# Performance work log

Measured on AMD Instinct MI355X. Metric: run time of the kernel, lower is better.

The kernel has to match this reference:

```python
import jax, jax.numpy as jnp
import numpy as np

N = 200000  # num nodes == num edges (edge_weight serves as both node feature and edge weight)
D_HID = 128
D_OUT = 2


def setup_inputs() -> dict:
    key = jax.random.key(0)
    ks = jax.random.split(key, 5)
    edge_index = jax.random.randint(ks[0], (2, N), 0, N, dtype=jnp.int64)
    edge_weight = jax.random.uniform(ks[1], (N,), dtype=jnp.float32)
    # Glorot-ish init for GCNConv linear layers (bias=True by default in PyG)
    W1 = jax.random.normal(ks[2], (1, D_HID), dtype=jnp.float32) * (1.0 / np.sqrt(1))
    W2 = jax.random.normal(ks[3], (D_HID, D_HID), dtype=jnp.float32) * (1.0 / np.sqrt(D_HID))
    W3 = jax.random.normal(ks[4], (D_HID, D_OUT), dtype=jnp.float32) * (1.0 / np.sqrt(D_HID))
    b1 = jnp.zeros((D_HID,), dtype=jnp.float32)
    b2 = jnp.zeros((D_HID,), dtype=jnp.float32)
    b3 = jnp.zeros((D_OUT,), dtype=jnp.float32)
    return {"edge_index": edge_index, "edge_weight": edge_weight,
            "W1": W1, "b1": b1, "W2": W2, "b2": b2, "W3": W3, "b3": b3}


def reference(edge_index, edge_weight, W1, b1, W2, b2, W3, b3):
    n = edge_weight.shape[0]
    src, dst = edge_index[0], edge_index[1]
    # GCN symmetric normalization with self-loops (PyG gcn_norm, fill_value=1.0)
    loops = jnp.arange(n)
    src_f = jnp.concatenate([src, loops])            # [2N]
    dst_f = jnp.concatenate([dst, loops])            # [2N]
    w_f = jnp.concatenate([edge_weight, jnp.ones((n,), edge_weight.dtype)])
    deg = jax.ops.segment_sum(w_f, dst_f, num_segments=n)
    dinv = jnp.where(deg > 0, deg ** -0.5, 0.0)
    norm = dinv[src_f] * w_f * dinv[dst_f]           # [2N], identical for all layers

    def conv(x, W, b):
        h = x @ W                                    # linear transform first (out <= in path)
        msg = h[src_f] * norm[:, None]               # gather + edge scale
        return jax.ops.segment_sum(msg, dst_f, num_segments=n) + b  # scatter-add aggregate

    x = edge_weight[:, None]                         # node features = edge weights, [N,1]
    x = jax.nn.relu(conv(x, W1, b1))
    x = jax.nn.relu(conv(x, W2, b2))
    x = jax.nn.relu(conv(x, W3, b3))
    return jax.nn.log_softmax(x, axis=1)
```

## Files before the change

### kernel.cpp

```cpp
#include <hip/hip_runtime.h>

#define NN 200000
#define NE 200000
#define DH 128

typedef float f32x4 __attribute__((ext_vector_type(4)));
typedef _Float16 f16x8 __attribute__((ext_vector_type(8)));
#define AS1 __attribute__((address_space(1)))
#define AS3 __attribute__((address_space(3)))

__device__ __forceinline__ unsigned pack2h(float a, float b) {
  unsigned short ua = __builtin_bit_cast(unsigned short, (_Float16)a);
  unsigned short ub = __builtin_bit_cast(unsigned short, (_Float16)b);
  return (unsigned)ua | ((unsigned)ub << 16);
}

__global__ void k_deg(const int* __restrict__ dst, const float* __restrict__ ew,
                      int* __restrict__ pdeg, int* __restrict__ rank,
                      const float* __restrict__ W2, unsigned* __restrict__ w2g) {
  int tid = threadIdx.x;
  int e = blockIdx.x * 256 + tid;
  if (e < NE) {
    int d = dst[e];
    int addend = __float2int_rn(ew[e] * 1048576.0f) | (1 << 26);
    int old = atomicAdd(&pdeg[d], addend);
    rank[e] = (int)(((unsigned)old) >> 26);
  }
  if (blockIdx.x < 32) {
    int gid = blockIdx.x * 256 + tid;
    int fkc = gid >> 8, l = (gid >> 2) & 63, dd = gid & 3;
    int n = (fkc >> 2) * 16 + (l & 15);
    int dwp = (fkc & 3) * 16 + (l >> 4) * 4 + dd;
    w2g[gid] = pack2h(W2[(2 * dwp) * DH + n], W2[(2 * dwp + 1) * DH + n]);
  }
}

__global__ void k_scan1(const int* __restrict__ pdeg, int* __restrict__ rowptr,
                        int* __restrict__ bsum) {
  __shared__ int sm[256];
  int tid = threadIdx.x;
  int i = blockIdx.x * 256 + tid;
  int v = (i < NN) ? (int)(((unsigned)pdeg[i]) >> 26) : 0;
  sm[tid] = v;
  __syncthreads();
  int x = v;
  for (int off = 1; off < 256; off <<= 1) {
    int y = (tid >= off) ? sm[tid - off] : 0;
    __syncthreads();
    x += y;
    sm[tid] = x;
    __syncthreads();
  }
  if (i < NN) rowptr[i] = x - v;
  if (tid == 255) bsum[blockIdx.x] = x;
}

__global__ void k_scan3(int* __restrict__ rowptr, const int* __restrict__ bsum,
                        const int* __restrict__ pdeg, const float* __restrict__ ew,
                        float* __restrict__ dinv, float* __restrict__ s) {
  __shared__ int sm[256];
  int tid = threadIdx.x;
  int partial = 0;
  for (int b = tid; b < blockIdx.x; b += 256) partial += bsum[b];
  sm[tid] = partial;
  __syncthreads();
  for (int off = 128; off; off >>= 1) {
    if (tid < off) sm[tid] += sm[tid + off];
    __syncthreads();
  }
  int boff = sm[0];
  int i = blockIdx.x * 256 + tid;
  if (i < NN) {
    rowptr[i] += boff;
    float deg = (float)(((unsigned)pdeg[i]) & 0x03FFFFFFu) * (1.0f / 1048576.0f) + 1.0f;
    float dv = rsqrtf(deg);
    dinv[i] = dv;
    s[i] = dv * dv * ew[i];
  }
  if (i == 0) rowptr[NN] = NE;
}

__global__ void k_scatter(const int* __restrict__ src, const int* __restrict__ dst,
                          const float* __restrict__ ew, const int* __restrict__ rank,
                          const float* __restrict__ dinv, const int* __restrict__ rowptr,
                          float* __restrict__ s, int2* __restrict__ epack) {
  int e = blockIdx.x * 256 + threadIdx.x;
  if (e < NE) {
    int si = src[e], di = dst[e];
    float nr = dinv[si] * ew[e] * dinv[di];
    int pos = rowptr[di] + rank[e];
    epack[pos] = make_int2(si, __float_as_int(nr));
    atomicAdd(&s[di], nr * ew[si]);
  }
}

__global__ __launch_bounds__(256, 3) void k_layer2(
    const float* __restrict__ s, const float* __restrict__ dinv,
    const int* __restrict__ rowptr, const int2* __restrict__ epack,
    const float* __restrict__ W1, const float* __restrict__ b1,
    const float* __restrict__ b2, const float* __restrict__ W3,
    const unsigned* __restrict__ w2g, float* __restrict__ h3) {
  __shared__ __align__(16) uint4 tAf[1024];
  __shared__ __align__(16) unsigned w2t[8192];
  __shared__ float eS[256], eN[256];
  int tid = threadIdx.x;
  int wv = tid >> 6;

#pragma unroll
  for (int i = 0; i < 8; ++i)
    __builtin_amdgcn_global_load_lds(
        (const AS1 unsigned*)(w2g + i * 1024 + tid * 4),
        (AS3 unsigned*)(w2t + i * 1024 + wv * 256), 16, 0, 0);

  int base = blockIdx.x * 64;
  int lr15 = tid & 15, q = (tid >> 4) & 3;
  int d = base + wv * 16 + lr15;
  float w1r[32], b1r[32];
#pragma unroll
  for (int c = 0; c < 32; c++) { w1r[c] = W1[q * 32 + c]; b1r[c] = b1[q * 32 + c]; }

  float sd = s[d], dv = dinv[d], sn = dv * dv;
  float acc[32];
#pragma unroll
  for (int c = 0; c < 32; c++)
    acc[c] = sn * fmaxf(fmaf(sd, w1r[c], b1r[c]), 0.f);

  int begd = rowptr[d], endd = rowptr[d + 1];
  int beg = rowptr[base], end = rowptr[base + 64];

  for (int cb = beg; cb < end; cb += 256) {
    int ce = min(cb + 256, end);
    __syncthreads();
    if (tid < ce - cb) {
      int2 ep = epack[cb + tid];
      eS[tid] = s[ep.x];
      eN[tid] = __int_as_float(ep.y);
    }
    __syncthreads();
    int jb = max(begd, cb), je = min(endd, ce);
    for (int j = jb; j < je; ++j) {
      float ss = eS[j - cb], nr = eN[j - cb];
#pragma unroll
      for (int c = 0; c < 32; c++)
        acc[c] = fmaf(nr, fmaxf(fmaf(ss, w1r[c], b1r[c]), 0.f), acc[c]);
    }
  }

#pragma unroll
  for (int hi = 0; hi < 4; ++hi) {
    uint4 u;
    u.x = pack2h(acc[8 * hi + 0], acc[8 * hi + 1]);
    u.y = pack2h(acc[8 * hi + 2], acc[8 * hi + 3]);
    u.z = pack2h(acc[8 * hi + 4], acc[8 * hi + 5]);
    u.w = pack2h(acc[8 * hi + 6], acc[8 * hi + 7]);
    tAf[(wv * 4 + q) * 64 + hi * 16 + lr15] = u;
  }
  __syncthreads();

  int l = tid & 63, g = l >> 4, lr = l & 15;
  f32x4 acc8[8];
#pragma unroll
  for (int f = 0; f < 8; f++) acc8[f] = (f32x4){0.f, 0.f, 0.f, 0.f};
#pragma unroll
  for (int kc = 0; kc < 4; kc++) {
    f16x8 av = __builtin_bit_cast(f16x8, tAf[(wv * 4 + kc) * 64 + l]);
#pragma unroll
    for (int f = 0; f < 8; f++) {
      f16x8 bv = __builtin_bit_cast(f16x8, *(const uint4*)(w2t + ((f * 4 + kc) * 64 + l) * 4));
      acc8[f] = __builtin_amdgcn_mfma_f32_16x16x32_f16(av, bv, acc8[f], 0, 0, 0);
    }
  }

  float p0[4] = {0.f, 0.f, 0.f, 0.f}, p1[4] = {0.f, 0.f, 0.f, 0.f};
#pragma unroll
  for (int f = 0; f < 8; f++) {
    int n = f * 16 + lr;
    float bb = b2[n];
    float2 w3v = ((const float2*)W3)[n];
#pragma unroll
    for (int r = 0; r < 4; r++) {
      float v = fmaxf(acc8[f][r] + bb, 0.f);
      p0[r] = fmaf(v, w3v.x, p0[r]);
      p1[r] = fmaf(v, w3v.y, p1[r]);
    }
  }
#pragma unroll
  for (int r = 0; r < 4; r++) {
#pragma unroll
    for (int m = 8; m; m >>= 1) {
      p0[r] += __shfl_xor(p0[r], m);
      p1[r] += __shfl_xor(p1[r], m);
    }
  }
  if (lr == 0) {
#pragma unroll
    for (int r = 0; r < 4; r++) {
      int node = base + wv * 16 + g * 4 + r;
      ((float2*)h3)[node] = make_float2(p0[r], p1[r]);
    }
  }
}

__global__ void k_final(const float* __restrict__ h3, const float* __restrict__ dinv,
                        const int* __restrict__ rowptr, const int2* __restrict__ epack,
                        const float* __restrict__ b3, float* __restrict__ out) {
  int d = blockIdx.x * 256 + threadIdx.x;
  if (d < NN) {
    float dv = dinv[d], sn = dv * dv;
    float2 hv = ((const float2*)h3)[d];
    float y0 = sn * hv.x, y1 = sn * hv.y;
    int beg = rowptr[d], end = rowptr[d + 1];
    for (int j = beg; j < end; ++j) {
      int2 ep = epack[j];
      float2 hs = ((const float2*)h3)[ep.x];
      float nr = __int_as_float(ep.y);
      y0 = fmaf(nr, hs.x, y0);
      y1 = fmaf(nr, hs.y, y1);
    }
    float z0 = fmaxf(y0 + b3[0], 0.f);
    float z1 = fmaxf(y1 + b3[1], 0.f);
    float m = fmaxf(z0, z1);
    float lse = m + logf(expf(z0 - m) + expf(z1 - m));
    out[2 * d] = z0 - lse;
    out[2 * d + 1] = z1 - lse;
  }
}

extern "C" void kernel_launch(void* const* d_in, const int* in_sizes, int n_in,
                              void* d_out, int out_size, void* d_ws, size_t ws_size,
                              hipStream_t stream) {
  const int* ei = (const int*)d_in[0];
  const int* srcp = ei;
  const int* dstp = ei + NE;
  const float* ew = (const float*)d_in[1];
  const float* W1 = (const float*)d_in[2];
  const float* b1 = (const float*)d_in[3];
  const float* W2 = (const float*)d_in[4];
  const float* b2 = (const float*)d_in[5];
  const float* W3 = (const float*)d_in[6];
  const float* b3 = (const float*)d_in[7];
  float* out = (float*)d_out;

  char* ws = (char*)d_ws;
  size_t off = 0;
  auto alloc = [&](size_t bytes) -> void* {
    void* p = ws + off;
    off = (off + bytes + 255) & ~size_t(255);
    return p;
  };
  int* pdeg = (int*)alloc(NN * 4);
  size_t zero_bytes = off;
  int* rank = (int*)alloc(NE * 4);
  float* s = (float*)alloc(NN * 4);
  float* dinv = (float*)alloc(NN * 4);
  int* rowptr = (int*)alloc((NN + 1) * 4);
  int* bsum = (int*)alloc(1024 * 4);
  int2* epack = (int2*)alloc(NE * 8);
  unsigned* w2g = (unsigned*)alloc(8192 * 4);
  float* h3 = (float*)alloc(NN * 2 * 4);
  (void)ws_size; (void)in_sizes; (void)n_in; (void)out_size;

  const int nbE = (NE + 255) / 256;
  const int nbN = (NN + 255) / 256;

  hipMemsetAsync(pdeg, 0, zero_bytes, stream);
  k_deg<<<nbE, 256, 0, stream>>>(dstp, ew, pdeg, rank, W2, w2g);
  k_scan1<<<nbN, 256, 0, stream>>>(pdeg, rowptr, bsum);
  k_scan3<<<nbN, 256, 0, stream>>>(rowptr, bsum, pdeg, ew, dinv, s);
  k_scatter<<<nbE, 256, 0, stream>>>(srcp, dstp, ew, rank, dinv, rowptr, s, epack);
  k_layer2<<<NN / 64, 256, 0, stream>>>(s, dinv, rowptr, epack, W1, b1, b2, W3, w2g, h3);
  k_final<<<nbN, 256, 0, stream>>>(h3, dinv, rowptr, epack, b3, out);
}
```

Measured before the change: 135.4 us.

## Fuse pipeline into one cooperative persistent kernel with grid syncs and tile tickets

Replaces the six-kernel chain (degree, two scan passes, scatter, layer2, final) with one cooperative kernel. It uses grid-wide syncs between phases and an atomic ticket for dynamic tile scheduling in the MFMA layer. The aim is to remove launch overhead and inter-kernel gaps on the mostly small phases. The cost is grid.sync overhead, a grid capped at 3 blocks per CU, and a naive per-chunk block-offset reduction in the scan phase that runs in quadratic time. The old multi-kernel path is kept as a fallback if the cooperative launch fails.

```diff
diff --git a/kernel.cpp b/kernel.cpp
--- a/kernel.cpp
+++ b/kernel.cpp
@@ -1,8 +1,13 @@
 #include <hip/hip_runtime.h>
+#include <hip/hip_cooperative_groups.h>
 
 #define NN 200000
 #define NE 200000
 #define DH 128
+#define NTILES (NN / 64)
+#define NCH ((NN + 255) / 256)
+
+namespace cg = cooperative_groups;
 
 typedef float f32x4 __attribute__((ext_vector_type(4)));
 typedef _Float16 f16x8 __attribute__((ext_vector_type(8)));
@@ -13,6 +18,216 @@
   unsigned short ua = __builtin_bit_cast(unsigned short, (_Float16)a);
   unsigned short ub = __builtin_bit_cast(unsigned short, (_Float16)b);
   return (unsigned)ua | ((unsigned)ub << 16);
+}
+
+__global__ __launch_bounds__(256, 3) void k_all(
+    const int* __restrict__ src, const int* __restrict__ dst,
+    const float* __restrict__ ew,
+    const float* __restrict__ W1, const float* __restrict__ b1,
+    const float* __restrict__ W2, const float* __restrict__ b2,
+    const float* __restrict__ W3, const float* __restrict__ b3,
+    float* __restrict__ out,
+    int* __restrict__ pdeg, int* __restrict__ ticket, int* __restrict__ rank,
+    float* __restrict__ s, float* __restrict__ dinv, int* __restrict__ rowptr,
+    int* __restrict__ agg, int2* __restrict__ epack,
+    unsigned* __restrict__ w2g, float* __restrict__ h3) {
+  cg::grid_group grid = cg::this_grid();
+  __shared__ __align__(16) char smem[51200];
+  uint4* tAf = (uint4*)smem;
+  unsigned* w2t = (unsigned*)(smem + 16384);
+  float* eS = (float*)(smem + 49152);
+  float* eN = (float*)(smem + 50176);
+  int* sm = (int*)smem;
+  __shared__ int s_tile;
+  int tid = threadIdx.x;
+  int gsz = gridDim.x * 256;
+  int gtid = blockIdx.x * 256 + tid;
+
+  for (int e = gtid; e < NE; e += gsz) {
+    int d = dst[e];
+    int addend = __float2int_rn(ew[e] * 1048576.0f) | (1 << 26);
+    int old = atomicAdd(&pdeg[d], addend);
+    rank[e] = (int)(((unsigned)old) >> 26);
+  }
+  for (int gid = gtid; gid < 8192; gid += gsz) {
+    int fkc = gid >> 8, l = (gid >> 2) & 63, dd = gid & 3;
+    int n = (fkc >> 2) * 16 + (l & 15);
+    int dwp = (fkc & 3) * 16 + (l >> 4) * 4 + dd;
+    w2g[gid] = pack2h(W2[(2 * dwp) * DH + n], W2[(2 * dwp + 1) * DH + n]);
+  }
+  grid.sync();
+
+  for (int c = blockIdx.x; c < NCH; c += gridDim.x) {
+    int i = c * 256 + tid;
+    int v = (i < NN) ? (int)(((unsigned)pdeg[i]) >> 26) : 0;
+    __syncthreads();
+    sm[tid] = v;
+    __syncthreads();
+    int x = v;
+    for (int off = 1; off < 256; off <<= 1) {
+      int y = (tid >= off) ? sm[tid - off] : 0;
+      __syncthreads();
+      x += y;
+      sm[tid] = x;
+      __syncthreads();
+    }
+    if (i < NN) rowptr[i] = x - v;
+    if (tid == 255) agg[c] = x;
+  }
+  grid.sync();
+
+  for (int c = blockIdx.x; c < NCH; c += gridDim.x) {
+    int partial = 0;
+    for (int j = tid; j < c; j += 256) partial += agg[j];
+    __syncthreads();
+    sm[tid] = partial;
+    __syncthreads();
+    for (int off = 128; off; off >>= 1) {
+      if (tid < off) sm[tid] += sm[tid + off];
+      __syncthreads();
+    }
+    int boff = sm[0];
+    int i = c * 256 + tid;
+    if (i < NN) {
+      rowptr[i] += boff;
+      float deg = (float)(((unsigned)pdeg[i]) & 0x03FFFFFFu) * (1.0f / 1048576.0f) + 1.0f;
+      float dv = rsqrtf(deg);
+      dinv[i] = dv;
+      s[i] = dv * dv * ew[i];
+    }
+  }
+  if (gtid == 0) rowptr[NN] = NE;
+  grid.sync();
+
+  for (int e = gtid; e < NE; e += gsz) {
+    int si = src[e], di = dst[e];
+    float nr = dinv[si] * ew[e] * dinv[di];
+    int pos = rowptr[di] + rank[e];
+    epack[pos] = make_int2(si, __float_as_int(nr));
+    atomicAdd(&s[di], nr * ew[si]);
+  }
+  grid.sync();
+
+  int wv = tid >> 6;
+#pragma unroll
+  for (int i = 0; i < 8; ++i)
+    __builtin_amdgcn_global_load_lds(
+        (const AS1 unsigned*)(w2g + i * 1024 + tid * 4),
+        (AS3 unsigned*)(w2t + i * 1024 + wv * 256), 16, 0, 0);
+  int lr15 = tid & 15, q = (tid >> 4) & 3;
+  float w1r[32], b1r[32];
+#pragma unroll
+  for (int c = 0; c < 32; c++) { w1r[c] = W1[q * 32 + c]; b1r[c] = b1[q * 32 + c]; }
+  int l = tid & 63, g = l >> 4, lr = l & 15;
+
+  for (;;) {
+    if (tid == 0) s_tile = atomicAdd(ticket, 1);
+    __syncthreads();
+    int tile = s_tile;
+    if (tile >= NTILES) break;
+    int base = tile * 64;
+    int d = base + wv * 16 + lr15;
+
+    float sd = s[d], dv = dinv[d], sn = dv * dv;
+    float acc[32];
+#pragma unroll
+    for (int c = 0; c < 32; c++)
+      acc[c] = sn * fmaxf(fmaf(sd, w1r[c], b1r[c]), 0.f);
+
+    int begd = rowptr[d], endd = rowptr[d + 1];
+    int beg = rowptr[base], end = rowptr[base + 64];
+    for (int cb = beg; cb < end; cb += 256) {
+      int ce = min(cb + 256, end);
+      __syncthreads();
+      if (tid < ce - cb) {
+        int2 ep = epack[cb + tid];
+        eS[tid] = s[ep.x];
+        eN[tid] = __int_as_float(ep.y);
+      }
+      __syncthreads();
+      int jb = max(begd, cb), je = min(endd, ce);
+      for (int j = jb; j < je; ++j) {
+        float ss = eS[j - cb], nr = eN[j - cb];
+#pragma unroll
+        for (int c = 0; c < 32; c++)
+          acc[c] = fmaf(nr, fmaxf(fmaf(ss, w1r[c], b1r[c]), 0.f), acc[c]);
+      }
+    }
+
+#pragma unroll
+    for (int hi = 0; hi < 4; ++hi) {
+      uint4 u;
+      u.x = pack2h(acc[8 * hi + 0], acc[8 * hi + 1]);
+      u.y = pack2h(acc[8 * hi + 2], acc[8 * hi + 3]);
+      u.z = pack2h(acc[8 * hi + 4], acc[8 * hi + 5]);
+      u.w = pack2h(acc[8 * hi + 6], acc[8 * hi + 7]);
+      tAf[(wv * 4 + q) * 64 + hi * 16 + lr15] = u;
+    }
+    __syncthreads();
+
+    f32x4 acc8[8];
+#pragma unroll
+    for (int f = 0; f < 8; f++) acc8[f] = (f32x4){0.f, 0.f, 0.f, 0.f};
+#pragma unroll
+    for (int kc = 0; kc < 4; kc++) {
+      f16x8 av = __builtin_bit_cast(f16x8, tAf[(wv * 4 + kc) * 64 + l]);
+#pragma unroll
+      for (int f = 0; f < 8; f++) {
+        f16x8 bv = __builtin_bit_cast(f16x8, *(const uint4*)(w2t + ((f * 4 + kc) * 64 + l) * 4));
+        acc8[f] = __builtin_amdgcn_mfma_f32_16x16x32_f16(av, bv, acc8[f], 0, 0, 0);
+      }
+    }
+
+    float p0[4] = {0.f, 0.f, 0.f, 0.f}, p1[4] = {0.f, 0.f, 0.f, 0.f};
+#pragma unroll
+    for (int f = 0; f < 8; f++) {
+      int n = f * 16 + lr;
+      float bb = b2[n];
+      float2 w3v = ((const float2*)W3)[n];
+#pragma unroll
+      for (int r = 0; r < 4; r++) {
+        float v = fmaxf(acc8[f][r] + bb, 0.f);
+        p0[r] = fmaf(v, w3v.x, p0[r]);
+        p1[r] = fmaf(v, w3v.y, p1[r]);
+      }
+    }
+#pragma unroll
+    for (int r = 0; r < 4; r++) {
+#pragma unroll
+      for (int m = 8; m; m >>= 1) {
+        p0[r] += __shfl_xor(p0[r], m);
+        p1[r] += __shfl_xor(p1[r], m);
+      }
+    }
+    if (lr == 0) {
+#pragma unroll
+      for (int r = 0; r < 4; r++) {
+        int node = base + wv * 16 + g * 4 + r;
+        ((float2*)h3)[node] = make_float2(p0[r], p1[r]);
+      }
+    }
+  }
+  grid.sync();
+
+  for (int d = gtid; d < NN; d += gsz) {
+    float dv = dinv[d], sn = dv * dv;
+    float2 hv = ((const float2*)h3)[d];
+    float y0 = sn * hv.x, y1 = sn * hv.y;
+    int beg = rowptr[d], end = rowptr[d + 1];
+    for (int j = beg; j < end; ++j) {
+      int2 ep = epack[j];
+      float2 hs = ((const float2*)h3)[ep.x];
+      float nr = __int_as_float(ep.y);
+      y0 = fmaf(nr, hs.x, y0);
+      y1 = fmaf(nr, hs.y, y1);
+    }
+    float z0 = fmaxf(y0 + b3[0], 0.f);
+    float z1 = fmaxf(y1 + b3[1], 0.f);
+    float m = fmaxf(z0, z1);
+    float lse = m + logf(expf(z0 - m) + expf(z1 - m));
+    out[2 * d] = z0 - lse;
+    out[2 * d + 1] = z1 - lse;
+  }
 }
 
 __global__ void k_deg(const int* __restrict__ dst, const float* __restrict__ ew,
@@ -105,29 +320,24 @@
   __shared__ float eS[256], eN[256];
   int tid = threadIdx.x;
   int wv = tid >> 6;
-
 #pragma unroll
   for (int i = 0; i < 8; ++i)
     __builtin_amdgcn_global_load_lds(
         (const AS1 unsigned*)(w2g + i * 1024 + tid * 4),
         (AS3 unsigned*)(w2t + i * 1024 + wv * 256), 16, 0, 0);
-
   int base = blockIdx.x * 64;
   int lr15 = tid & 15, q = (tid >> 4) & 3;
   int d = base + wv * 16 + lr15;
   float w1r[32], b1r[32];
 #pragma unroll
   for (int c = 0; c < 32; c++) { w1r[c] = W1[q * 32 + c]; b1r[c] = b1[q * 32 + c]; }
-
   float sd = s[d], dv = dinv[d], sn = dv * dv;
   float acc[32];
 #pragma unroll
   for (int c = 0; c < 32; c++)
     acc[c] = sn * fmaxf(fmaf(sd, w1r[c], b1r[c]), 0.f);
-
   int begd = rowptr[d], endd = rowptr[d + 1];
   int beg = rowptr[base], end = rowptr[base + 64];
-
   for (int cb = beg; cb < end; cb += 256) {
     int ce = min(cb + 256, end);
     __syncthreads();
@@ -145,7 +355,6 @@
         acc[c] = fmaf(nr, fmaxf(fmaf(ss, w1r[c], b1r[c]), 0.f), acc[c]);
     }
   }
-
 #pragma unroll
   for (int hi = 0; hi < 4; ++hi) {
     uint4 u;
@@ -156,7 +365,6 @@
     tAf[(wv * 4 + q) * 64 + hi * 16 + lr15] = u;
   }
   __syncthreads();
-
   int l = tid & 63, g = l >> 4, lr = l & 15;
   f32x4 acc8[8];
 #pragma unroll
@@ -170,7 +378,6 @@
       acc8[f] = __builtin_amdgcn_mfma_f32_16x16x32_f16(av, bv, acc8[f], 0, 0, 0);
     }
   }
-
   float p0[4] = {0.f, 0.f, 0.f, 0.f}, p1[4] = {0.f, 0.f, 0.f, 0.f};
 #pragma unroll
   for (int f = 0; f < 8; f++) {
@@ -249,25 +456,41 @@
     return p;
   };
   int* pdeg = (int*)alloc(NN * 4);
+  int* ticket = (int*)alloc(256 * 4);
   size_t zero_bytes = off;
   int* rank = (int*)alloc(NE * 4);
   float* s = (float*)alloc(NN * 4);
   float* dinv = (float*)alloc(NN * 4);
   int* rowptr = (int*)alloc((NN + 1) * 4);
-  int* bsum = (int*)alloc(1024 * 4);
+  int* agg = (int*)alloc(1024 * 4);
   int2* epack = (int2*)alloc(NE * 8);
   unsigned* w2g = (unsigned*)alloc(8192 * 4);
   float* h3 = (float*)alloc(NN * 2 * 4);
   (void)ws_size; (void)in_sizes; (void)n_in; (void)out_size;
 
-  const int nbE = (NE + 255) / 256;
-  const int nbN = (NN + 255) / 256;
-
   hipMemsetAsync(pdeg, 0, zero_bytes, stream);
-  k_deg<<<nbE, 256, 0, stream>>>(dstp, ew, pdeg, rank, W2, w2g);
-  k_scan1<<<nbN, 256, 0, stream>>>(pdeg, rowptr, bsum);
-  k_scan3<<<nbN, 256, 0, stream>>>(rowptr, bsum, pdeg, ew, dinv, s);
-  k_scatter<<<nbE, 256, 0, stream>>>(srcp, dstp, ew, rank, dinv, rowptr, s, epack);
-  k_layer2<<<NN / 64, 256, 0, stream>>>(s, dinv, rowptr, epack, W1, b1, b2, W3, w2g, h3);
-  k_final<<<nbN, 256, 0, stream>>>(h3, dinv, rowptr, epack, b3, out);
-}
+
+  int occ = 0;
+  hipError_t oe = hipOccupancyMaxActiveBlocksPerMultiprocessor(&occ, k_all, 256, 0);
+  if (oe != hipSuccess || occ < 1) occ = 1;
+  if (occ > 3) occ = 3;
+  int G = occ * 256;
+
+  void* args[] = {
+      (void*)&srcp, (void*)&dstp, (void*)&ew, (void*)&W1, (void*)&b1,
+      (void*)&W2, (void*)&b2, (void*)&W3, (void*)&b3, (void*)&out,
+      (void*)&pdeg, (void*)&ticket, (void*)&rank, (void*)&s, (void*)&dinv,
+      (void*)&rowptr, (void*)&agg, (void*)&epack, (void*)&w2g, (void*)&h3};
+  hipError_t rc = hipLaunchCooperativeKernel(k_all, dim3(G), dim3(256), args, 0, stream);
+
+  if (rc != hipSuccess) {
+    const int nbE = (NE + 255) / 256;
+    const int nbN = (NN + 255) / 256;
+    k_deg<<<nbE, 256, 0, stream>>>(dstp, ew, pdeg, rank, W2, w2g);
+    k_scan1<<<nbN, 256, 0, stream>>>(pdeg, rowptr, agg);
+    k_scan3<<<nbN, 256, 0, stream>>>(rowptr, agg, pdeg, ew, dinv, s);
+    k_scatter<<<nbE, 256, 0, stream>>>(srcp, dstp, ew, rank, dinv, rowptr, s, epack);
+    k_layer2<<<NN / 64, 256, 0, stream>>>(s, dinv, rowptr, epack, W1, b1, b2, W3, w2g, h3);
+    k_final<<<nbN, 256, 0, stream>>>(h3, dinv, rowptr, epack, b3, out);
+  }
+}
```

Measured after the change: 321.6 us. 2.38x slower.
